# Kernel optimization log

Hardware: AMD Instinct MI355X
Metric: run time of the kernel (lower is better)

Reference implementation:

```python
import jax, jax.numpy as jnp
import numpy as np

N = 12288
E = 393216
D_IN, D_HID, D_OUT = 128, 128, 64


def gcn_conv(x, edge_index, W, b, num_nodes):
    # PyG GCNConv: h = x @ W; add self-loops; sym-normalize; scatter-add; + b
    h = x @ W  # [N, F]
    row, col = edge_index[0], edge_index[1]
    sl = jnp.arange(num_nodes, dtype=edge_index.dtype)
    row = jnp.concatenate([row, sl])
    col = jnp.concatenate([col, sl])
    deg = jax.ops.segment_sum(jnp.ones_like(col, dtype=h.dtype), col, num_segments=num_nodes)
    dinv = jax.lax.rsqrt(jnp.maximum(deg, 1e-12))
    norm = dinv[row] * dinv[col]  # [E+N]
    msgs = h[row] * norm[:, None]
    out = jax.ops.segment_sum(msgs, col, num_segments=num_nodes)
    return out + b


def setup_inputs() -> dict:
    key = jax.random.key(0)
    k1, k2, k3, k4, k5 = jax.random.split(key, 5)
    x = jax.random.uniform(k1, (N, D_IN), dtype=jnp.float32)
    edge_index = jax.random.randint(k2, (2, E), 0, N, dtype=jnp.int64)
    # Glorot-style init for GCN weights, zeros for biases (PyG defaults)
    W1 = jax.random.normal(k3, (D_IN, D_HID), dtype=jnp.float32) * (1.0 / np.sqrt(D_IN))
    b1 = jnp.zeros((D_HID,), dtype=jnp.float32)
    W2 = jax.random.normal(k4, (D_HID, D_OUT), dtype=jnp.float32) * (1.0 / np.sqrt(D_HID))
    b2 = jnp.zeros((D_OUT,), dtype=jnp.float32)
    return {"x": x, "edge_index": edge_index, "W1": W1, "b1": b1, "W2": W2, "b2": b2}


def reference(x, edge_index, W1, b1, W2, b2):
    h = jax.nn.relu(gcn_conv(x, edge_index, W1, b1, N))
    latent = gcn_conv(h, edge_index, W2, b2, N)  # [N, D_OUT]
    return latent @ latent.T  # [N, N] gram-matrix decoder
```

## Files before the change

kernel.cpp:

```cpp
#include <hip/hip_runtime.h>

#define NN   12288
#define EE   393216
#define DIN  128
#define DHID 128
#define DOUT 64
#define CAP  96

typedef __attribute__((ext_vector_type(8))) short bf16x8;
typedef __attribute__((ext_vector_type(4))) float f32x4;
typedef __attribute__((ext_vector_type(4))) short s16x4;

__device__ __forceinline__ short f2bf(float f) {
    unsigned u = __float_as_uint(f);
    unsigned r = (u + 0x7fffu + ((u >> 16) & 1u)) >> 16;
    return (short)r;
}
__device__ __forceinline__ float bf2f(short h) {
    return __uint_as_float(((unsigned)(unsigned short)h) << 16);
}

#define GEMM1_BLOCKS 768
#define FILL_BLOCKS  512
__global__ __launch_bounds__(256) void k_fill_gemm1(const float* __restrict__ x,
                                                    const int* __restrict__ row,
                                                    const int* __restrict__ col,
                                                    const float* __restrict__ W1,
                                                    unsigned* __restrict__ cursor,
                                                    int* __restrict__ bucket,
                                                    float* __restrict__ g1) {
    const int b = blockIdx.x, t = threadIdx.x;
    if (b < GEMM1_BLOCKS) {
        __shared__ float xs[16 * DIN];
        const int r0 = b * 16;
        for (int j = t; j < 16 * DIN; j += 256) xs[j] = x[(size_t)r0 * DIN + j];
        __syncthreads();
        const int c = t & 127, rg = (t >> 7) * 8;
        float acc[8] = {};
        for (int k = 0; k < DIN; ++k) {
            float w = W1[k * DHID + c];
#pragma unroll
            for (int r = 0; r < 8; ++r) acc[r] += xs[(rg + r) * DIN + k] * w;
        }
#pragma unroll
        for (int r = 0; r < 8; ++r) g1[(size_t)(r0 + rg + r) * DHID + c] = acc[r];
    } else {
        const int gid = (b - GEMM1_BLOCKS) * 256 + t;
#pragma unroll
        for (int q = 0; q < 3; ++q) {
            int e = gid + q * (FILL_BLOCKS * 256);
            int c = col[e];
            unsigned p = atomicAdd(&cursor[c], 1u);
            if (p < CAP) bucket[(size_t)c * CAP + p] = row[e];
        }
    }
}

__global__ __launch_bounds__(256) void k_gather1_gemm2(const float* __restrict__ g1,
                                                       const int* __restrict__ bucket,
                                                       const unsigned* __restrict__ cursor,
                                                       const float* __restrict__ b1,
                                                       const float* __restrict__ W2,
                                                       float* __restrict__ g2) {
    __shared__ float hs[4][DHID];
    const int lane = threadIdx.x & 63, wave = threadIdx.x >> 6;
    const int c = blockIdx.x * 4 + wave;
    const unsigned cnt = cursor[c];
    const float dc = rsqrtf((float)cnt + 1.0f);
    const unsigned e = cnt < CAP ? cnt : CAP;
    const f32x4* __restrict__ G4 = (const f32x4*)g1;
    const int* __restrict__ bk = bucket + (size_t)c * CAP;
    const int sub = lane >> 5, col4 = lane & 31;

    f32x4 acc = (f32x4){0.f, 0.f, 0.f, 0.f};
    if (sub == 0) acc = G4[(size_t)c * 32 + col4] * dc;

    unsigned i = 0;
    for (; i + 8 <= e; i += 8) {
        int r[4];
        float d[4];
        f32x4 v[4];
#pragma unroll
        for (int p = 0; p < 4; ++p) {
            r[p] = bk[i + 2 * p + sub];
            d[p] = rsqrtf((float)cursor[r[p]] + 1.0f);
            v[p] = G4[(size_t)r[p] * 32 + col4];
        }
#pragma unroll
        for (int p = 0; p < 4; ++p) acc += v[p] * d[p];
    }
    for (; i + 2 <= e; i += 2) {
        int rr = bk[i + sub];
        float d = rsqrtf((float)cursor[rr] + 1.0f);
        acc += G4[(size_t)rr * 32 + col4] * d;
    }
    if (i < e && sub == 0) {
        int rr = bk[i];
        float d = rsqrtf((float)cursor[rr] + 1.0f);
        acc += G4[(size_t)rr * 32 + col4] * d;
    }
    acc.x += __shfl_xor(acc.x, 32);
    acc.y += __shfl_xor(acc.y, 32);
    acc.z += __shfl_xor(acc.z, 32);
    acc.w += __shfl_xor(acc.w, 32);

    f32x4 bb = ((const f32x4*)b1)[col4];
    f32x4 o = acc * dc + bb;
    o.x = fmaxf(o.x, 0.f);
    o.y = fmaxf(o.y, 0.f);
    o.z = fmaxf(o.z, 0.f);
    o.w = fmaxf(o.w, 0.f);
    if (sub == 0) ((f32x4*)hs[wave])[col4] = o;

    float a2 = 0.f;
#pragma unroll 8
    for (int k = 0; k < DHID; ++k) a2 += hs[wave][k] * W2[k * DOUT + lane];
    g2[(size_t)c * DOUT + lane] = a2 * dc;
}

__global__ __launch_bounds__(256) void k_gather2(const float* __restrict__ g2,
                                                 const int* __restrict__ bucket,
                                                 const unsigned* __restrict__ cursor,
                                                 const float* __restrict__ b2,
                                                 short* __restrict__ H,
                                                 short* __restrict__ Lo) {
    const int lane = threadIdx.x & 63, wave = threadIdx.x >> 6;
    const int c = blockIdx.x * 4 + wave;
    const unsigned cnt = cursor[c];
    const float dc = rsqrtf((float)cnt + 1.0f);
    const unsigned e = cnt < CAP ? cnt : CAP;
    const f32x4* __restrict__ G4 = (const f32x4*)g2;
    const int* __restrict__ bk = bucket + (size_t)c * CAP;
    const int sub = lane >> 4, col4 = lane & 15;

    f32x4 acc = (f32x4){0.f, 0.f, 0.f, 0.f};
    if (sub == 0) acc = G4[(size_t)c * 16 + col4];

    unsigned i = 0;
    for (; i + 8 <= e; i += 8) {
        int r0 = bk[i + sub], r1 = bk[i + 4 + sub];
        f32x4 v0 = G4[(size_t)r0 * 16 + col4];
        f32x4 v1 = G4[(size_t)r1 * 16 + col4];
        acc += v0;
        acc += v1;
    }
    for (; i + 4 <= e; i += 4) {
        int rr = bk[i + sub];
        acc += G4[(size_t)rr * 16 + col4];
    }
    if (i < e) {
        if (sub < (int)(e - i)) {
            int rr = bk[i + sub];
            acc += G4[(size_t)rr * 16 + col4];
        }
    }
    acc.x += __shfl_xor(acc.x, 16); acc.x += __shfl_xor(acc.x, 32);
    acc.y += __shfl_xor(acc.y, 16); acc.y += __shfl_xor(acc.y, 32);
    acc.z += __shfl_xor(acc.z, 16); acc.z += __shfl_xor(acc.z, 32);
    acc.w += __shfl_xor(acc.w, 16); acc.w += __shfl_xor(acc.w, 32);

    if (sub == 0) {
        f32x4 bb = ((const f32x4*)b2)[col4];
        f32x4 v = acc * dc + bb;
        s16x4 h4, l4;
        h4.x = f2bf(v.x); l4.x = f2bf(v.x - bf2f(h4.x));
        h4.y = f2bf(v.y); l4.y = f2bf(v.y - bf2f(h4.y));
        h4.z = f2bf(v.z); l4.z = f2bf(v.z - bf2f(h4.z));
        h4.w = f2bf(v.w); l4.w = f2bf(v.w - bf2f(h4.w));
        ((s16x4*)H)[(size_t)c * 16 + col4] = h4;
        ((s16x4*)Lo)[(size_t)c * 16 + col4] = l4;
    }
}

#define NTILE 96
#define NPAIR ((NTILE * (NTILE + 1)) / 2)
__global__ __launch_bounds__(256) void k_gram(const short* __restrict__ H,
                                              const short* __restrict__ L,
                                              float* __restrict__ out) {
    __shared__ float P[128][132];
    const int tid  = threadIdx.x;
    const int lane = tid & 63;
    const int wave = tid >> 6;

    const int Lb = blockIdx.x;
    int bi = (int)((193.0f - sqrtf(193.0f * 193.0f - 8.0f * (float)Lb)) * 0.5f);
    if (bi < 0) bi = 0;
    if (bi > NTILE - 1) bi = NTILE - 1;
    while (bi * NTILE - (bi * (bi - 1)) / 2 > Lb) --bi;
    while ((bi + 1) * NTILE - ((bi + 1) * bi) / 2 <= Lb) ++bi;
    const int bj = bi + (Lb - (bi * NTILE - (bi * (bi - 1)) / 2));

    const int wm = wave >> 1, wn = wave & 1;
    const int row0 = bi * 128 + wm * 64;
    const int col0 = bj * 128 + wn * 64;
    const int fr = lane & 15;
    const int fk = (lane >> 4) << 3;
    const int crow = (lane >> 4) * 4;
    const bool mirror = (bi != bj);

    bf16x8 aH[4][2], aL[4][2];
#pragma unroll
    for (int m = 0; m < 4; ++m)
#pragma unroll
        for (int k = 0; k < 2; ++k) {
            size_t off = (size_t)(row0 + m * 16 + fr) * DOUT + k * 32 + fk;
            aH[m][k] = *(const bf16x8*)(H + off);
            aL[m][k] = *(const bf16x8*)(L + off);
        }

#pragma unroll
    for (int n = 0; n < 4; ++n) {
        bf16x8 bH[2], bL[2];
#pragma unroll
        for (int k = 0; k < 2; ++k) {
            size_t off = (size_t)(col0 + n * 16 + fr) * DOUT + k * 32 + fk;
            bH[k] = *(const bf16x8*)(H + off);
            bL[k] = *(const bf16x8*)(L + off);
        }
        f32x4 acc[4];
#pragma unroll
        for (int m = 0; m < 4; ++m) acc[m] = (f32x4){0.f, 0.f, 0.f, 0.f};

#pragma unroll
        for (int m = 0; m < 4; ++m)
#pragma unroll
            for (int k = 0; k < 2; ++k) {
                acc[m] = __builtin_amdgcn_mfma_f32_16x16x32_bf16(aL[m][k], bH[k], acc[m], 0, 0, 0);
                acc[m] = __builtin_amdgcn_mfma_f32_16x16x32_bf16(aH[m][k], bL[k], acc[m], 0, 0, 0);
                acc[m] = __builtin_amdgcn_mfma_f32_16x16x32_bf16(aH[m][k], bH[k], acc[m], 0, 0, 0);
            }

#pragma unroll
        for (int m = 0; m < 4; ++m)
#pragma unroll
            for (int j = 0; j < 4; ++j)
                P[wm * 64 + m * 16 + crow + j][wn * 64 + n * 16 + fr] = acc[m][j];
    }
    __syncthreads();

    const size_t gr0 = (size_t)bi * 128, gc0 = (size_t)bj * 128;
#pragma unroll
    for (int it = 0; it < 16; ++it) {
        int idx = it * 256 + tid;
        int r = idx >> 5, c4 = (idx & 31) << 2;
        f32x4 v = *(const f32x4*)&P[r][c4];
        __builtin_nontemporal_store(v, (f32x4*)&out[(gr0 + r) * NN + gc0 + c4]);
    }
    if (mirror) {
#pragma unroll
        for (int it = 0; it < 16; ++it) {
            int idx = it * 256 + tid;
            int r = idx >> 5, c4 = (idx & 31) << 2;
            f32x4 v;
            v.x = P[c4 + 0][r];
            v.y = P[c4 + 1][r];
            v.z = P[c4 + 2][r];
            v.w = P[c4 + 3][r];
            __builtin_nontemporal_store(v, (f32x4*)&out[(gc0 + r) * NN + gr0 + c4]);
        }
    }
}

extern "C" void kernel_launch(void* const* d_in, const int* in_sizes, int n_in,
                              void* d_out, int out_size, void* d_ws, size_t ws_size,
                              hipStream_t stream) {
    const float* x  = (const float*)d_in[0];
    const int*   ei = (const int*)d_in[1];
    const float* W1 = (const float*)d_in[2];
    const float* b1 = (const float*)d_in[3];
    const float* W2 = (const float*)d_in[4];
    const float* b2 = (const float*)d_in[5];
    float* out = (float*)d_out;

    const int* row = ei;
    const int* col = ei + EE;

    char* w = (char*)d_ws;
    unsigned* cursor = (unsigned*)w; w += (size_t)NN * 4;
    int*      bucket = (int*)w;      w += (size_t)NN * CAP * 4;
    float*    g1     = (float*)w;    w += (size_t)NN * DHID * 4;
    float*    g2     = (float*)w;    w += (size_t)NN * DOUT * 4;
    short*    latH   = (short*)w;    w += (size_t)NN * DOUT * 2;
    short*    latL   = (short*)w;    w += (size_t)NN * DOUT * 2;

    hipMemsetAsync(cursor, 0, (size_t)NN * 4, stream);

    k_fill_gemm1<<<GEMM1_BLOCKS + FILL_BLOCKS, 256, 0, stream>>>(x, row, col, W1, cursor, bucket, g1);
    k_gather1_gemm2<<<NN / 4, 256, 0, stream>>>(g1, bucket, cursor, b1, W2, g2);
    k_gather2<<<NN / 4, 256, 0, stream>>>(g2, bucket, cursor, b2, latH, latL);

    k_gram<<<NPAIR, 256, 0, stream>>>(latH, latL, out);
}
```

Measured before the change: 213.2 us.

## Halve gram LDS staging tile and software-prefetch bucket indices in aggregations

The gram kernel now keeps all 16 accumulator fragments in registers and stages the 128x128 output through a 64-row LDS buffer in two halves. This halves shared memory per block so more blocks can be resident while the output stores stream out, at the cost of extra accumulator registers and extra barriers. Both aggregation kernels also load the next iteration's neighbour indices one step ahead, shortening the dependent load chain behind each gather.

```diff
diff --git a/kernel.cpp b/kernel.cpp
--- a/kernel.cpp
+++ b/kernel.cpp
@@ -76,18 +76,30 @@
     if (sub == 0) acc = G4[(size_t)c * 32 + col4] * dc;
 
     unsigned i = 0;
-    for (; i + 8 <= e; i += 8) {
+    int pr[4];
+    if (i + 8 <= e) {
+#pragma unroll
+        for (int p = 0; p < 4; ++p) pr[p] = bk[i + 2 * p + sub];
+    }
+    for (; i + 8 <= e;) {
         int r[4];
+#pragma unroll
+        for (int p = 0; p < 4; ++p) r[p] = pr[p];
+        const unsigned ni = i + 8;
+        if (ni + 8 <= e) {
+#pragma unroll
+            for (int p = 0; p < 4; ++p) pr[p] = bk[ni + 2 * p + sub];
+        }
         float d[4];
         f32x4 v[4];
 #pragma unroll
         for (int p = 0; p < 4; ++p) {
-            r[p] = bk[i + 2 * p + sub];
             d[p] = rsqrtf((float)cursor[r[p]] + 1.0f);
             v[p] = G4[(size_t)r[p] * 32 + col4];
         }
 #pragma unroll
         for (int p = 0; p < 4; ++p) acc += v[p] * d[p];
+        i = ni;
     }
     for (; i + 2 <= e; i += 2) {
         int rr = bk[i + sub];
@@ -137,12 +149,17 @@
     if (sub == 0) acc = G4[(size_t)c * 16 + col4];
 
     unsigned i = 0;
-    for (; i + 8 <= e; i += 8) {
-        int r0 = bk[i + sub], r1 = bk[i + 4 + sub];
+    int pr0 = 0, pr1 = 0;
+    if (i + 8 <= e) { pr0 = bk[i + sub]; pr1 = bk[i + 4 + sub]; }
+    for (; i + 8 <= e;) {
+        int r0 = pr0, r1 = pr1;
+        const unsigned ni = i + 8;
+        if (ni + 8 <= e) { pr0 = bk[ni + sub]; pr1 = bk[ni + 4 + sub]; }
         f32x4 v0 = G4[(size_t)r0 * 16 + col4];
         f32x4 v1 = G4[(size_t)r1 * 16 + col4];
         acc += v0;
         acc += v1;
+        i = ni;
     }
     for (; i + 4 <= e; i += 4) {
         int rr = bk[i + sub];
@@ -177,7 +194,7 @@
 __global__ __launch_bounds__(256) void k_gram(const short* __restrict__ H,
                                               const short* __restrict__ L,
                                               float* __restrict__ out) {
-    __shared__ float P[128][132];
+    __shared__ float P[64][132];
     const int tid  = threadIdx.x;
     const int lane = tid & 63;
     const int wave = tid >> 6;
@@ -208,6 +225,12 @@
             aL[m][k] = *(const bf16x8*)(L + off);
         }
 
+    f32x4 acc[4][4];
+#pragma unroll
+    for (int n = 0; n < 4; ++n)
+#pragma unroll
+        for (int m = 0; m < 4; ++m) acc[n][m] = (f32x4){0.f, 0.f, 0.f, 0.f};
+
 #pragma unroll
     for (int n = 0; n < 4; ++n) {
         bf16x8 bH[2], bL[2];
@@ -217,46 +240,49 @@
             bH[k] = *(const bf16x8*)(H + off);
             bL[k] = *(const bf16x8*)(L + off);
         }
-        f32x4 acc[4];
-#pragma unroll
-        for (int m = 0; m < 4; ++m) acc[m] = (f32x4){0.f, 0.f, 0.f, 0.f};
-
 #pragma unroll
         for (int m = 0; m < 4; ++m)
 #pragma unroll
             for (int k = 0; k < 2; ++k) {
-                acc[m] = __builtin_amdgcn_mfma_f32_16x16x32_bf16(aL[m][k], bH[k], acc[m], 0, 0, 0);
-                acc[m] = __builtin_amdgcn_mfma_f32_16x16x32_bf16(aH[m][k], bL[k], acc[m], 0, 0, 0);
-                acc[m] = __builtin_amdgcn_mfma_f32_16x16x32_bf16(aH[m][k], bH[k], acc[m], 0, 0, 0);
+                acc[n][m] = __builtin_amdgcn_mfma_f32_16x16x32_bf16(aL[m][k], bH[k], acc[n][m], 0, 0, 0);
+                acc[n][m] = __builtin_amdgcn_mfma_f32_16x16x32_bf16(aH[m][k], bL[k], acc[n][m], 0, 0, 0);
+                acc[n][m] = __builtin_amdgcn_mfma_f32_16x16x32_bf16(aH[m][k], bH[k], acc[n][m], 0, 0, 0);
             }
-
-#pragma unroll
-        for (int m = 0; m < 4; ++m)
-#pragma unroll
-            for (int j = 0; j < 4; ++j)
-                P[wm * 64 + m * 16 + crow + j][wn * 64 + n * 16 + fr] = acc[m][j];
-    }
-    __syncthreads();
+    }
 
     const size_t gr0 = (size_t)bi * 128, gc0 = (size_t)bj * 128;
 #pragma unroll
-    for (int it = 0; it < 16; ++it) {
-        int idx = it * 256 + tid;
-        int r = idx >> 5, c4 = (idx & 31) << 2;
-        f32x4 v = *(const f32x4*)&P[r][c4];
-        __builtin_nontemporal_store(v, (f32x4*)&out[(gr0 + r) * NN + gc0 + c4]);
-    }
-    if (mirror) {
-#pragma unroll
-        for (int it = 0; it < 16; ++it) {
+    for (int h = 0; h < 2; ++h) {
+        __syncthreads();
+        if (wm == h) {
+#pragma unroll
+            for (int n = 0; n < 4; ++n)
+#pragma unroll
+                for (int m = 0; m < 4; ++m)
+#pragma unroll
+                    for (int j = 0; j < 4; ++j)
+                        P[m * 16 + crow + j][wn * 64 + n * 16 + fr] = acc[n][m][j];
+        }
+        __syncthreads();
+#pragma unroll
+        for (int it = 0; it < 8; ++it) {
             int idx = it * 256 + tid;
             int r = idx >> 5, c4 = (idx & 31) << 2;
-            f32x4 v;
-            v.x = P[c4 + 0][r];
-            v.y = P[c4 + 1][r];
-            v.z = P[c4 + 2][r];
-            v.w = P[c4 + 3][r];
-            __builtin_nontemporal_store(v, (f32x4*)&out[(gc0 + r) * NN + gr0 + c4]);
+            f32x4 v = *(const f32x4*)&P[r][c4];
+            __builtin_nontemporal_store(v, (f32x4*)&out[(gr0 + h * 64 + r) * NN + gc0 + c4]);
+        }
+        if (mirror) {
+#pragma unroll
+            for (int it = 0; it < 8; ++it) {
+                int idx = it * 256 + tid;
+                int r = idx >> 4, c4 = (idx & 15) << 2;
+                f32x4 v;
+                v.x = P[c4 + 0][r];
+                v.y = P[c4 + 1][r];
+                v.z = P[c4 + 2][r];
+                v.w = P[c4 + 3][r];
+                __builtin_nontemporal_store(v, (f32x4*)&out[(gc0 + r) * NN + gr0 + h * 64 + c4]);
+            }
         }
     }
 }
```

Measured after the change: 207.9 us (median of 2 runs). -2.5%, faster.
